# Kernel optimization log

Hardware: AMD Instinct MI355X
Metric: run time of the kernel (lower is better)

Reference implementation:

```python
import jax, jax.numpy as jnp
import numpy as np

N_NODES, IN_CH, T_IN = 2048, 64, 512
CONV_F, LSTM_H = 64, 128
NEG_BIG = -9.0e15


def conv1d(x, w, b):
    # x: [N, C_in, T], w: [C_out, C_in, 3], padding=1
    y = jax.lax.conv_general_dilated(x, w, window_strides=(1,), padding=((1, 1),),
                                     dimension_numbers=('NCH', 'OIH', 'NCH'))
    return y + b[None, :, None]


def batchnorm(x, g, b, eps=1e-5):
    # training-mode BatchNorm1d: batch stats over (N, T) per channel, biased var
    m = x.mean(axis=(0, 2), keepdims=True)
    v = x.var(axis=(0, 2), keepdims=True)
    return g[None, :, None] * (x - m) / jnp.sqrt(v + eps) + b[None, :, None]


def maxpool2(x):
    n, c, t = x.shape
    return x.reshape(n, c, t // 2, 2).max(axis=-1)


def lstm_dir(x, w_ih, w_hh, b):
    # x: [T, N, D]; gate order i, f, g, o (PyTorch convention)
    T, N, _ = x.shape
    H = w_hh.shape[1]
    pre = jnp.einsum('tnd,gd->tng', x, w_ih) + b  # [T, N, 4H]
    def step(carry, p):
        h, c = carry
        gates = p + h @ w_hh.T
        i, f, g, o = jnp.split(gates, 4, axis=-1)
        c = jax.nn.sigmoid(f) * c + jax.nn.sigmoid(i) * jnp.tanh(g)
        h = jax.nn.sigmoid(o) * jnp.tanh(c)
        return (h, c), h
    init = (jnp.zeros((N, H), x.dtype), jnp.zeros((N, H), x.dtype))
    _, hs = jax.lax.scan(step, init, pre)
    return hs  # [T, N, H]


def gat_layer(h, adj, W, a):
    # e[i,j] = leakyrelu(a . [Wh_i, Wh_j]) computed without the NxNx2F concat
    Wh = h @ W.T                      # [N, F]
    F_ = Wh.shape[1]
    s1 = Wh @ a[0, :F_]               # contribution of target node i
    s2 = Wh @ a[0, F_:]               # contribution of source node j
    e = jax.nn.leaky_relu(s1[:, None] + s2[None, :], 0.2)
    att = jax.nn.softmax(jnp.where(adj > 0, e, NEG_BIG), axis=1)
    return att @ Wh


def setup_inputs() -> dict:
    key = jax.random.key(0)
    ks = jax.random.split(key, 24)
    s = 0.05
    f32 = jnp.float32
    inp = {
        'x': jax.random.normal(ks[0], (N_NODES, IN_CH, T_IN), f32),
        'adj': jax.random.randint(ks[1], (N_NODES, N_NODES), 0, 2, jnp.int32),
        'conv1_w': s * jax.random.normal(ks[2], (CONV_F, IN_CH, 3), f32),
        'conv1_b': s * jax.random.normal(ks[3], (CONV_F,), f32),
        'bn1_g': jnp.ones((CONV_F,), f32),
        'bn1_b': jnp.zeros((CONV_F,), f32),
        'conv2_w': s * jax.random.normal(ks[4], (2 * CONV_F, CONV_F, 3), f32),
        'conv2_b': s * jax.random.normal(ks[5], (2 * CONV_F,), f32),
        'bn2_g': jnp.ones((2 * CONV_F,), f32),
        'bn2_b': jnp.zeros((2 * CONV_F,), f32),
        'wif': s * jax.random.normal(ks[6], (4 * LSTM_H, 2 * CONV_F), f32),
        'whf': s * jax.random.normal(ks[7], (4 * LSTM_H, LSTM_H), f32),
        'bf': s * jax.random.normal(ks[8], (4 * LSTM_H,), f32),
        'wir': s * jax.random.normal(ks[9], (4 * LSTM_H, 2 * CONV_F), f32),
        'whr': s * jax.random.normal(ks[10], (4 * LSTM_H, LSTM_H), f32),
        'br': s * jax.random.normal(ks[11], (4 * LSTM_H,), f32),
        'gat1_W': s * jax.random.normal(ks[12], (128, 256), f32),
        'gat1_a': s * jax.random.normal(ks[13], (1, 256), f32),
        'gat2_W': s * jax.random.normal(ks[14], (128, 128), f32),
        'gat2_a': s * jax.random.normal(ks[15], (1, 256), f32),
    }
    return inp


def reference(x, adj, conv1_w, conv1_b, bn1_g, bn1_b, conv2_w, conv2_b, bn2_g, bn2_b,
              wif, whf, bf, wir, whr, br, gat1_W, gat1_a, gat2_W, gat2_a):
    y = maxpool2(jax.nn.relu(batchnorm(conv1d(x, conv1_w, conv1_b), bn1_g, bn1_b)))
    y = maxpool2(jax.nn.relu(batchnorm(conv1d(y, conv2_w, conv2_b), bn2_g, bn2_b)))
    seq = y.transpose(2, 0, 1)                 # [T, N, 2*conv_filters]
    hf = lstm_dir(seq, wif, whf, bf)           # [T, N, H]
    hr = lstm_dir(seq[::-1], wir, whr, br)[::-1]
    feats = jnp.concatenate([hf, hr], axis=-1).mean(axis=0)  # [N, 256]
    h1 = jax.nn.elu(gat_layer(feats, adj, gat1_W, gat1_a))
    return gat_layer(h1, adj, gat2_W, gat2_a)
```

## Files before the change

kernel.cpp:

```cpp
#include <hip/hip_runtime.h>

typedef unsigned int uint;
#define DI __device__ __forceinline__

typedef __bf16 bf16;
typedef __attribute__((ext_vector_type(4))) float f32x4;
typedef __attribute__((ext_vector_type(8))) __bf16 bf16x8;
typedef __attribute__((ext_vector_type(4))) int i32x4;

constexpr size_t OFF_A    = 0;
constexpr size_t OFF_B    = 33554432;
constexpr size_t OFF_B1   = OFF_B + 16777216;
constexpr size_t OFF_WHHG = 67108864;
constexpr size_t OFF_WIHG = OFF_WHHG + 65536;
constexpr size_t OFF_BIAS = OFF_WIHG + 65536;
constexpr size_t OFF_HSUM = OFF_BIAS + 1024;
constexpr size_t OFF_FEAT = OFF_HSUM + 524288;
constexpr size_t OFF_WH1  = OFF_FEAT + 524288;
constexpr size_t OFF_S1A  = OFF_WH1 + 262144;
constexpr size_t OFF_S2A  = OFF_S1A + 2048;
constexpr size_t OFF_H1   = OFF_S2A + 2048;
constexpr size_t OFF_WH2  = OFF_H1 + 262144;
constexpr size_t OFF_S1B  = OFF_WH2 + 262144;
constexpr size_t OFF_S2B  = OFF_S1B + 2048;
constexpr size_t OFF_STAT = OFF_S2B + 2048;
constexpr size_t OFF_W1P  = OFF_STAT + 512;
constexpr size_t OFF_W2P  = OFF_W1P + 6144;
constexpr size_t OFF_WHT  = OFF_W2P + 12288;
constexpr size_t OFF_STATP= OFF_WHT + 131072;

DI float bflo(uint u){ union { uint i; float f; } v; v.i = u << 16;         return v.f; }
DI float bfhi(uint u){ union { uint i; float f; } v; v.i = u & 0xffff0000u; return v.f; }
DI float fexp2_(float x){ return __builtin_amdgcn_exp2f(x); }
DI float frcp_(float x){ return __builtin_amdgcn_rcpf(x); }
DI float sigf_(float x){ return frcp_(1.0f + fexp2_(x * -1.44269504f)); }
DI float tanhx_(float x){ return 1.0f - 2.0f*frcp_(1.0f + fexp2_(x * 2.88539009f)); }

DI f32x4 mfma16(i32x4 a, i32x4 b, f32x4 c){
  return __builtin_amdgcn_mfma_f32_16x16x32_bf16(
      __builtin_bit_cast(bf16x8, a), __builtin_bit_cast(bf16x8, b), c, 0, 0, 0);
}

DI char* swz128(char* base, int row, int byteInRow){ return base + row*128 + (byteInRow ^ ((row&7)<<4)); }
DI char* swz256(char* base, int row, int byteInRow){ return base + row*256 + (byteInRow ^ ((row&7)<<4)); }

__global__ void prep_kernel(const float* __restrict__ whf, const float* __restrict__ whr,
                            const float* __restrict__ wif, const float* __restrict__ wir,
                            const float* __restrict__ bfv, const float* __restrict__ brv,
                            const float* __restrict__ c1w, const float* __restrict__ c2w,
                            bf16* __restrict__ whh_g, bf16* __restrict__ wih_g,
                            float* __restrict__ bias_g,
                            bf16* __restrict__ w1p, bf16* __restrict__ w2p)
{
  const int dir = blockIdx.y;
  const float* whh = dir ? whr : whf;
  const float* wih = dir ? wir : wif;
  const float* bb  = dir ? brv : bfv;
  int idx = blockIdx.x*256 + threadIdx.x;
  int c = idx >> 7, d = idx & 127;
  int src = ((c & 3)*128 + (c >> 2))*128 + d;
  whh_g[(size_t)dir*65536 + idx] = (bf16)whh[src];
  wih_g[(size_t)dir*65536 + idx] = (bf16)wih[src];
  if (idx < 512) bias_g[dir*512 + idx] = bb[(idx & 3)*128 + (idx >> 2)];
  if (dir == 0) {
    if (idx < 12288) {
      int row = idx >> 6;
      int ci = (((idx & 63)*2) ^ ((row & 7) << 4)) >> 1;
      int co = row & 63, dk = row >> 6;
      w1p[idx] = (bf16)c1w[(co*64 + ci)*3 + dk];
    }
    if (idx < 24576) {
      int row = idx >> 6;
      int ci = (((idx & 63)*2) ^ ((row & 7) << 4)) >> 1;
      int co = row & 127, dk = row >> 7;
      w2p[idx] = (bf16)c2w[(co*64 + ci)*3 + dk];
    }
  }
}

__global__ __launch_bounds__(512) void conv1_kernel(
    const float* __restrict__ x, const bf16* __restrict__ w1p,
    const float* __restrict__ bias, bf16* __restrict__ y, float* __restrict__ statp)
{
  __shared__ bf16 xa[2][16512];
  __shared__ bf16 wb[12288];
  __shared__ float redS[64], redQ[64];
  const int tid = threadIdx.x, nb = blockIdx.x*8;
  {
    const i32x4* wsrc = (const i32x4*)w1p;
    for (int i = tid; i < 1536; i += 512) ((i32x4*)wb)[i] = wsrc[i];
    if (tid < 64) { redS[tid] = 0.f; redQ[tid] = 0.f; }
  }
  auto stage = [&](int buf, int n, int t0) {
    char* base = (char*)xa[buf];
    for (int i = tid; i < 2048; i += 512) {
      int q = i & 63, cp = i >> 6;
      int ci = cp*2;
      const float* xb = &x[((size_t)n*64 + ci)*512 + t0 + q*4];
      float4 v0 = *(const float4*)xb;
      float4 v1 = *(const float4*)(xb + 512);
      int row = q*4 + 1;
      union { bf16 h[2]; uint u; } p0, p1, p2, p3;
      p0.h[0]=(bf16)v0.x; p0.h[1]=(bf16)v1.x;
      p1.h[0]=(bf16)v0.y; p1.h[1]=(bf16)v1.y;
      p2.h[0]=(bf16)v0.z; p2.h[1]=(bf16)v1.z;
      p3.h[0]=(bf16)v0.w; p3.h[1]=(bf16)v1.w;
      *(uint*)swz128(base, row+0, ci*2) = p0.u;
      *(uint*)swz128(base, row+1, ci*2) = p1.u;
      *(uint*)swz128(base, row+2, ci*2) = p2.u;
      *(uint*)swz128(base, row+3, ci*2) = p3.u;
    }
    if (tid < 128) {
      int ci = tid >> 1, e = tid & 1;
      int row = e ? 257 : 0;
      int t = t0 + (e ? 256 : -1);
      float v = (t >= 0 && t < 512) ? x[((size_t)n*64 + ci)*512 + t] : 0.0f;
      *(bf16*)swz128(base, row, ci*2) = (bf16)v;
    }
  };
  stage(0, nb, 0);
  __syncthreads();
  const int lane = tid & 63, wv = tid >> 6;
  const int m0 = (wv & 3)*64, c0 = (wv >> 2)*32;
  const int l15 = lane & 15, lh = lane >> 4;
  const float bb0 = bias[c0 + l15], bb1 = bias[c0 + 16 + l15];
  float bnS[2] = {0.f,0.f}, bnQ[2] = {0.f,0.f};
  for (int it = 0; it < 16; ++it) {
    const int n = nb + (it >> 1), t0 = (it & 1)*256, buf = it & 1;
    if (it + 1 < 16) stage(buf ^ 1, nb + ((it + 1) >> 1), ((it + 1) & 1)*256);
    char* xb = (char*)xa[buf];
    f32x4 acc[4][2];
    #pragma unroll
    for (int mf = 0; mf < 4; ++mf) {
      acc[mf][0] = (f32x4){bb0, bb0, bb0, bb0};
      acc[mf][1] = (f32x4){bb1, bb1, bb1, bb1};
    }
    #pragma unroll
    for (int dk = 0; dk < 3; ++dk)
      #pragma unroll
      for (int ks = 0; ks < 2; ++ks) {
        const int kb = ks*64 + lh*16;
        i32x4 bfr[2], afr[4];
        #pragma unroll
        for (int cf = 0; cf < 2; ++cf) {
          int row = dk*64 + c0 + cf*16 + l15;
          bfr[cf] = *(const i32x4*)swz128((char*)wb, row, kb);
        }
        #pragma unroll
        for (int mf = 0; mf < 4; ++mf) {
          int row = m0 + mf*16 + l15 + dk;
          afr[mf] = *(const i32x4*)swz128(xb, row, kb);
        }
        #pragma unroll
        for (int mf = 0; mf < 4; ++mf)
          #pragma unroll
          for (int cf = 0; cf < 2; ++cf)
            acc[mf][cf] = mfma16(afr[mf], bfr[cf], acc[mf][cf]);
      }
    #pragma unroll
    for (int mf = 0; mf < 4; ++mf)
      #pragma unroll
      for (int cf = 0; cf < 2; ++cf) {
        int co = c0 + cf*16 + l15;
        int tt = t0 + m0 + mf*16 + lh*4;
        union { bf16 h[4]; uint2 u; } pk;
        #pragma unroll
        for (int r = 0; r < 4; ++r) {
          float v = acc[mf][cf][r];
          pk.h[r] = (bf16)v;
          bnS[cf] += v; bnQ[cf] += v*v;
        }
        *(uint2*)&y[((size_t)n*64 + co)*512 + tt] = pk.u;
      }
    __syncthreads();
  }
  atomicAdd(&redS[c0 + l15], bnS[0]);      atomicAdd(&redQ[c0 + l15], bnQ[0]);
  atomicAdd(&redS[c0 + 16 + l15], bnS[1]); atomicAdd(&redQ[c0 + 16 + l15], bnQ[1]);
  __syncthreads();
  if (tid < 64) {
    float* row = statp + (size_t)(blockIdx.x & 31)*256;
    atomicAdd(&row[tid], redS[tid]);
    atomicAdd(&row[128 + tid], redQ[tid]);
  }
}

__global__ __launch_bounds__(512) void conv2_kernel(
    const bf16* __restrict__ xin, const bf16* __restrict__ w2p,
    const float* __restrict__ bias, bf16* __restrict__ y, float* __restrict__ statp)
{
  __shared__ bf16 xa[2][16512];
  __shared__ bf16 wb[24576];
  __shared__ float redS[128], redQ[128];
  const int tid = threadIdx.x, nb = blockIdx.x*8;
  {
    const i32x4* wsrc = (const i32x4*)w2p;
    for (int i = tid; i < 3072; i += 512) ((i32x4*)wb)[i] = wsrc[i];
    if (tid < 128) { redS[tid] = 0.f; redQ[tid] = 0.f; }
    if (tid < 256) {
      int ci = (tid & 127) >> 1, e = tid & 1, buf = tid >> 7;
      int row = e ? 257 : 0;
      *(bf16*)swz128((char*)xa[buf], row, ci*2) = (bf16)0.0f;
    }
  }
  auto stage = [&](int buf, int n) {
    char* base = (char*)xa[buf];
    const i32x4* src = (const i32x4*)(xin + (size_t)n*16384);
    for (int i = tid; i < 2048; i += 512) {
      int row = (i >> 3) + 1, blk = i & 7;
      *(i32x4*)swz128(base, row, blk*16) = src[i];
    }
  };
  stage(0, nb);
  __syncthreads();
  const int lane = tid & 63, wv = tid >> 6;
  const int m0 = (wv & 3)*64, c0 = (wv >> 2)*64;
  const int l15 = lane & 15, lh = lane >> 4;
  float bbv[4];
  #pragma unroll
  for (int cf = 0; cf < 4; ++cf) bbv[cf] = bias[c0 + cf*16 + l15];
  float bnS[4] = {0.f,0.f,0.f,0.f}, bnQ[4] = {0.f,0.f,0.f,0.f};
  for (int it = 0; it < 8; ++it) {
    const int n = nb + it, buf = it & 1;
    if (it + 1 < 8) stage(buf ^ 1, nb + it + 1);
    char* xb = (char*)xa[buf];
    f32x4 acc[4][4];
    #pragma unroll
    for (int mf = 0; mf < 4; ++mf)
      #pragma unroll
      for (int cf = 0; cf < 4; ++cf)
        acc[mf][cf] = (f32x4){bbv[cf], bbv[cf], bbv[cf], bbv[cf]};
    #pragma unroll
    for (int dk = 0; dk < 3; ++dk)
      #pragma unroll
      for (int ks = 0; ks < 2; ++ks) {
        const int kb = ks*64 + lh*16;
        i32x4 bfr[4], afr[4];
        #pragma unroll
        for (int cf = 0; cf < 4; ++cf) {
          int row = dk*128 + c0 + cf*16 + l15;
          bfr[cf] = *(const i32x4*)swz128((char*)wb, row, kb);
        }
        #pragma unroll
        for (int mf = 0; mf < 4; ++mf) {
          int row = m0 + mf*16 + l15 + dk;
          afr[mf] = *(const i32x4*)swz128(xb, row, kb);
        }
        #pragma unroll
        for (int mf = 0; mf < 4; ++mf)
          #pragma unroll
          for (int cf = 0; cf < 4; ++cf)
            acc[mf][cf] = mfma16(afr[mf], bfr[cf], acc[mf][cf]);
      }
    #pragma unroll
    for (int mf = 0; mf < 4; ++mf)
      #pragma unroll
      for (int cf = 0; cf < 4; ++cf) {
        int co = c0 + cf*16 + l15;
        int tt = m0 + mf*16 + lh*4;
        union { bf16 h[4]; uint2 u; } pk;
        #pragma unroll
        for (int r = 0; r < 4; ++r) {
          float v = acc[mf][cf][r];
          pk.h[r] = (bf16)v;
          bnS[cf] += v; bnQ[cf] += v*v;
        }
        *(uint2*)&y[((size_t)n*128 + co)*256 + tt] = pk.u;
      }
    __syncthreads();
  }
  #pragma unroll
  for (int cf = 0; cf < 4; ++cf) {
    int co = c0 + cf*16 + l15;
    atomicAdd(&redS[co], bnS[cf]);
    atomicAdd(&redQ[co], bnQ[cf]);
  }
  __syncthreads();
  if (tid < 128) {
    float* row = statp + (size_t)(blockIdx.x & 31)*256;
    atomicAdd(&row[tid], redS[tid]);
    atomicAdd(&row[128 + tid], redQ[tid]);
  }
}

__global__ void bn_finalize_kernel(const float* __restrict__ statp, float* __restrict__ stat,
                                   const float* __restrict__ g, const float* __restrict__ b,
                                   int C, float invCnt)
{
  int c = threadIdx.x;
  if (c < C) {
    float s = 0.f, q = 0.f;
    for (int r = 0; r < 32; ++r) { s += statp[r*256 + c]; q += statp[r*256 + 128 + c]; }
    float m  = s*invCnt;
    float v  = q*invCnt - m*m;
    float sc = g[c]*rsqrtf(v + 1e-5f);
    stat[256+c] = sc;
    stat[384+c] = b[c] - m*sc;
  }
}

template<int C, int TH>
__global__ __launch_bounds__(256) void poolT_kernel(
    const bf16* __restrict__ yin, const float* __restrict__ stat, bf16* __restrict__ outp)
{
  __shared__ bf16 buf[C][TH + 2];
  const int n = blockIdx.x, tid = threadIdx.x;
  const uint* src = (const uint*)(yin + (size_t)n*C*TH*2);
  for (int i = tid; i < C*TH; i += 256) {
    int th = i & (TH - 1), c = i / TH;
    uint u = src[i];
    float sc = stat[256 + c], sh = stat[384 + c];
    float a = fmaxf(sc*bflo(u) + sh, 0.f);
    float b = fmaxf(sc*bfhi(u) + sh, 0.f);
    buf[c][th] = (bf16)fmaxf(a, b);
  }
  __syncthreads();
  bf16* dst = outp + (size_t)n*TH*C;
  for (int i = tid; i < TH*C/2; i += 256) {
    int cp = i & (C/2 - 1), th = i / (C/2);
    union { bf16 h[2]; uint u; } pk;
    pk.h[0] = buf[2*cp][th]; pk.h[1] = buf[2*cp + 1][th];
    *(uint*)&dst[th*C + 2*cp] = pk.u;
  }
}

__global__ __launch_bounds__(512, 2) void lstm_fused_kernel(
    const bf16* __restrict__ p2t, const bf16* __restrict__ wih_g,
    const bf16* __restrict__ whh_g, const float* __restrict__ bias_g,
    float* __restrict__ hsum)
{
  __shared__ bf16 hb[2][2048];
  const int z = blockIdx.x;
  const int dir = z & 1, n0 = (z >> 1)*16;
  const int tid = threadIdx.x, lane = tid & 63, wv = tid >> 6;
  const int l15 = lane & 15, lh = lane >> 4;
  i32x4 wihr[4][4], whhr[4][4];
  {
    const bf16* wi = wih_g + (size_t)dir*65536;
    const bf16* wh = whh_g + (size_t)dir*65536;
    #pragma unroll
    for (int cf = 0; cf < 4; ++cf) {
      int c = wv*64 + cf*16 + l15;
      #pragma unroll
      for (int ks = 0; ks < 4; ++ks) {
        wihr[cf][ks] = *(const i32x4*)(wi + (size_t)c*128 + ks*32 + lh*8);
        whhr[cf][ks] = *(const i32x4*)(wh + (size_t)c*128 + ks*32 + lh*8);
      }
    }
  }
  f32x4 bias4[4];
  #pragma unroll
  for (int cf = 0; cf < 4; ++cf) {
    int hh = wv*16 + cf*4 + lh;
    bias4[cf] = *(const f32x4*)&bias_g[dir*512 + hh*4];
  }
  for (int i = tid; i < 256; i += 512) ((i32x4*)hb[0])[i] = (i32x4){0,0,0,0};
  const bf16* xrow = p2t + (size_t)(n0 + l15)*128*128;
  float creg[4] = {0.f,0.f,0.f,0.f}, hac[4] = {0.f,0.f,0.f,0.f};
  f32x4 acc[4];
  i32x4 xn[4];
  {
    int ts0 = dir ? 127 : 0;
    #pragma unroll
    for (int ks = 0; ks < 4; ++ks)
      xn[ks] = *(const i32x4*)(xrow + (size_t)ts0*128 + ks*32 + lh*8);
    #pragma unroll
    for (int cf = 0; cf < 4; ++cf) {
      acc[cf] = mfma16(wihr[cf][0], xn[0], bias4[cf]);
      #pragma unroll
      for (int ks = 1; ks < 4; ++ks)
        acc[cf] = mfma16(wihr[cf][ks], xn[ks], acc[cf]);
    }
  }
  int cur = 0;
  __syncthreads();
  for (int t = 0; t < 128; ++t) {
    {
      int tn = (t + 1 < 128) ? t + 1 : 127;
      int tsn = dir ? 127 - tn : tn;
      #pragma unroll
      for (int ks = 0; ks < 4; ++ks)
        xn[ks] = *(const i32x4*)(xrow + (size_t)tsn*128 + ks*32 + lh*8);
    }
    {
      i32x4 a0 = *(const i32x4*)swz256((char*)hb[cur], l15, 0*64 + lh*16);
      i32x4 a1 = *(const i32x4*)swz256((char*)hb[cur], l15, 1*64 + lh*16);
      #pragma unroll
      for (int cf = 0; cf < 4; ++cf) {
        acc[cf] = mfma16(whhr[cf][0], a0, acc[cf]);
        acc[cf] = mfma16(whhr[cf][1], a1, acc[cf]);
      }
      a0 = *(const i32x4*)swz256((char*)hb[cur], l15, 2*64 + lh*16);
      a1 = *(const i32x4*)swz256((char*)hb[cur], l15, 3*64 + lh*16);
      #pragma unroll
      for (int cf = 0; cf < 4; ++cf) {
        acc[cf] = mfma16(whhr[cf][2], a0, acc[cf]);
        acc[cf] = mfma16(whhr[cf][3], a1, acc[cf]);
      }
    }
    #pragma unroll
    for (int cf = 0; cf < 4; ++cf) {
      float ig = sigf_(acc[cf][0]);
      float fg = sigf_(acc[cf][1]);
      float gg = tanhx_(acc[cf][2]);
      float og = sigf_(acc[cf][3]);
      float cv = fg*creg[cf] + ig*gg;
      creg[cf] = cv;
      float hv = og*tanhx_(cv);
      hac[cf] += hv;
      int hh = wv*16 + cf*4 + lh;
      *(bf16*)swz256((char*)hb[cur^1], l15, hh*2) = (bf16)hv;
    }
    #pragma unroll
    for (int cf = 0; cf < 4; ++cf) {
      acc[cf] = mfma16(wihr[cf][0], xn[0], bias4[cf]);
      #pragma unroll
      for (int ks = 1; ks < 4; ++ks)
        acc[cf] = mfma16(wihr[cf][ks], xn[ks], acc[cf]);
    }
    __syncthreads();
    cur ^= 1;
  }
  float* hm = hsum + ((size_t)dir*2048 + n0)*128;
  #pragma unroll
  for (int cf = 0; cf < 4; ++cf) {
    int hh = wv*16 + cf*4 + lh;
    hm[(size_t)l15*128 + hh] = hac[cf];
  }
}

__global__ __launch_bounds__(256) void feats_kernel(const float* __restrict__ hsum, float* __restrict__ feats)
{
  int idx = blockIdx.x*256 + threadIdx.x;
  int k = idx & 255, n = idx >> 8;
  float v = (k < 128) ? hsum[(size_t)n*128 + k]
                      : hsum[(size_t)2048*128 + (size_t)n*128 + (k - 128)];
  feats[idx] = v * 0.0078125f;
}

template<int K>
__global__ __launch_bounds__(256) void node_gemm_kernel(
    const float* __restrict__ inp, const float* __restrict__ W,
    float* __restrict__ outp, bf16* __restrict__ outT)
{
  __shared__ float ft[32][K];
  const int i0 = blockIdx.x*32, tid = threadIdx.x;
  for (int i = tid; i < 32*K; i += 256) ft[i/K][i%K] = inp[(size_t)i0*K + i];
  __syncthreads();
  const int f = tid & 127, ih = (tid >> 7)*16;
  float acc[16];
  #pragma unroll
  for (int ii = 0; ii < 16; ++ii) acc[ii] = 0.f;
  const float* wp = W + (size_t)f*K;
  for (int k = 0; k < K; k += 4) {
    const float4 wv = *reinterpret_cast<const float4*>(&wp[k]);
    #pragma unroll
    for (int ii = 0; ii < 16; ++ii) {
      const float* fp = &ft[ih+ii][k];
      acc[ii] += fp[0]*wv.x + fp[1]*wv.y + fp[2]*wv.z + fp[3]*wv.w;
    }
  }
  union { bf16 h[16]; uint4 u[2]; } pk;
  #pragma unroll
  for (int ii = 0; ii < 16; ++ii) {
    outp[(size_t)(i0+ih+ii)*128 + f] = acc[ii];
    pk.h[ii] = (bf16)acc[ii];
  }
  uint4* dT = (uint4*)&outT[(size_t)f*2048 + i0 + ih];
  dT[0] = pk.u[0]; dT[1] = pk.u[1];
}

__global__ __launch_bounds__(256) void gat_s_kernel(const float* __restrict__ Wh,
    const float* __restrict__ a, float* __restrict__ s1, float* __restrict__ s2)
{
  const int node = blockIdx.x*4 + (threadIdx.x >> 6);
  const int l = threadIdx.x & 63;
  const float w0 = Wh[(size_t)node*128 + l], w1 = Wh[(size_t)node*128 + 64 + l];
  float v1 = w0*a[l]     + w1*a[64+l];
  float v2 = w0*a[128+l] + w1*a[192+l];
  #pragma unroll
  for (int off = 32; off > 0; off >>= 1) { v1 += __shfl_down(v1, off); v2 += __shfl_down(v2, off); }
  if (l == 0) { s1[node] = v1; s2[node] = v2; }
}

__global__ __launch_bounds__(512) void gat_attn8_kernel(
    const bf16* __restrict__ WhT,
    const float* __restrict__ s1, const float* __restrict__ s2v,
    const int* __restrict__ adj, float* __restrict__ outp, int applyElu)
{
  __shared__ bf16 P[8*2048];
  __shared__ float sums[8];
  const int i0 = blockIdx.x*8, tid = threadIdx.x;
  const int lane = tid & 63, w = tid >> 6;
  {
    const int r = w, i = i0 + r;
    const float s1i = s1[i];
    const int4* arow = (const int4*)(adj + (size_t)i*2048);
    float ev[8][4];
    float m = -3.0e38f;
    #pragma unroll
    for (int k = 0; k < 8; ++k) {
      int4 ad = arow[k*64 + lane];
      float4 sv = *(const float4*)&s2v[k*256 + lane*4];
      float e0 = s1i + sv.x; e0 = (e0 > 0.f) ? e0 : 0.2f*e0; e0 = (ad.x > 0) ? e0 : -3.0e38f;
      float e1 = s1i + sv.y; e1 = (e1 > 0.f) ? e1 : 0.2f*e1; e1 = (ad.y > 0) ? e1 : -3.0e38f;
      float e2 = s1i + sv.z; e2 = (e2 > 0.f) ? e2 : 0.2f*e2; e2 = (ad.z > 0) ? e2 : -3.0e38f;
      float e3 = s1i + sv.w; e3 = (e3 > 0.f) ? e3 : 0.2f*e3; e3 = (ad.w > 0) ? e3 : -3.0e38f;
      ev[k][0]=e0; ev[k][1]=e1; ev[k][2]=e2; ev[k][3]=e3;
      m = fmaxf(m, fmaxf(fmaxf(e0,e1), fmaxf(e2,e3)));
    }
    #pragma unroll
    for (int off = 32; off > 0; off >>= 1) m = fmaxf(m, __shfl_xor(m, off));
    float s = 0.f;
    char* prow = (char*)P + r*4096;
    #pragma unroll
    for (int k = 0; k < 8; ++k) {
      float p0 = __expf(ev[k][0] - m);
      float p1 = __expf(ev[k][1] - m);
      float p2 = __expf(ev[k][2] - m);
      float p3 = __expf(ev[k][3] - m);
      s += (p0+p1)+(p2+p3);
      union { bf16 h[4]; uint2 u; } pk;
      pk.h[0]=(bf16)p0; pk.h[1]=(bf16)p1; pk.h[2]=(bf16)p2; pk.h[3]=(bf16)p3;
      *(uint2*)(prow + ((k*512 + lane*8) ^ ((r&7)<<4))) = pk.u;
    }
    #pragma unroll
    for (int off = 32; off > 0; off >>= 1) s += __shfl_xor(s, off);
    if (lane == 0) sums[r] = s;
  }
  __syncthreads();
  const int l15 = lane & 15, lh = lane >> 4;
  const int pr = l15 & 7;
  const bf16* bT = WhT + (size_t)(w*16 + l15)*2048;
  f32x4 ac[4];
  #pragma unroll
  for (int q = 0; q < 4; ++q) ac[q] = (f32x4){0.f,0.f,0.f,0.f};
  for (int kt = 0; kt < 64; kt += 4) {
    #pragma unroll
    for (int q = 0; q < 4; ++q) {
      i32x4 af = *(const i32x4*)((char*)P + pr*4096 + (((kt+q)*64 + lh*16) ^ ((pr&7)<<4)));
      i32x4 bf = *(const i32x4*)(bT + (kt+q)*32 + lh*8);
      ac[q] = mfma16(af, bf, ac[q]);
    }
  }
  f32x4 accv = (ac[0] + ac[1]) + (ac[2] + ac[3]);
  if (lh < 2) {
    #pragma unroll
    for (int rg = 0; rg < 4; ++rg) {
      int row = lh*4 + rg;
      float v = accv[rg] / sums[row];
      if (applyElu) v = (v > 0.f) ? v : (__expf(v) - 1.0f);
      outp[(size_t)(i0 + row)*128 + w*16 + l15] = v;
    }
  }
}

extern "C" void kernel_launch(void* const* d_in, const int* in_sizes, int n_in,
                              void* d_out, int out_size, void* d_ws, size_t ws_size,
                              hipStream_t stream)
{
  (void)in_sizes; (void)n_in; (void)out_size; (void)ws_size;
  const float* x    = (const float*)d_in[0];
  const int*   adj  = (const int*)d_in[1];
  const float* c1w  = (const float*)d_in[2];
  const float* c1b  = (const float*)d_in[3];
  const float* bn1g = (const float*)d_in[4];
  const float* bn1b = (const float*)d_in[5];
  const float* c2w  = (const float*)d_in[6];
  const float* c2b  = (const float*)d_in[7];
  const float* bn2g = (const float*)d_in[8];
  const float* bn2b = (const float*)d_in[9];
  const float* wif  = (const float*)d_in[10];
  const float* whf  = (const float*)d_in[11];
  const float* bfv  = (const float*)d_in[12];
  const float* wir  = (const float*)d_in[13];
  const float* whr  = (const float*)d_in[14];
  const float* brv  = (const float*)d_in[15];
  const float* g1W  = (const float*)d_in[16];
  const float* g1a  = (const float*)d_in[17];
  const float* g2W  = (const float*)d_in[18];
  const float* g2a  = (const float*)d_in[19];
  float* outp = (float*)d_out;
  float* ws   = (float*)d_ws;

  bf16* y12    = (bf16*)(ws + OFF_A);
  bf16* pool1t = (bf16*)(ws + OFF_B);
  bf16* pool2t = (bf16*)(ws + OFF_B1);
  bf16* whh_g  = (bf16*)(ws + OFF_WHHG);
  bf16* wih_g  = (bf16*)(ws + OFF_WIHG);
  float* bias_g= ws + OFF_BIAS;
  float* hsm   = ws + OFF_HSUM;
  float* feats = ws + OFF_FEAT;
  float* Wh1   = ws + OFF_WH1;
  float* s1a   = ws + OFF_S1A;
  float* s2a   = ws + OFF_S2A;
  float* h1    = ws + OFF_H1;
  float* Wh2   = ws + OFF_WH2;
  float* s1b   = ws + OFF_S1B;
  float* s2b   = ws + OFF_S2B;
  float* stat  = ws + OFF_STAT;
  bf16* w1p    = (bf16*)(ws + OFF_W1P);
  bf16* w2p    = (bf16*)(ws + OFF_W2P);
  bf16* whT    = (bf16*)(ws + OFF_WHT);
  float* statp = ws + OFF_STATP;

  prep_kernel<<<dim3(256,2),256,0,stream>>>(whf, whr, wif, wir, bfv, brv, c1w, c2w,
                                            whh_g, wih_g, bias_g, w1p, w2p);

  hipMemsetAsync(statp, 0, 8192*sizeof(float), stream);
  conv1_kernel<<<256,512,0,stream>>>(x, w1p, c1b, y12, statp);
  bn_finalize_kernel<<<1,128,0,stream>>>(statp, stat, bn1g, bn1b, 64, 1.0f/(2048.0f*512.0f));
  poolT_kernel<64,256><<<2048,256,0,stream>>>(y12, stat, pool1t);

  hipMemsetAsync(statp, 0, 8192*sizeof(float), stream);
  conv2_kernel<<<256,512,0,stream>>>(pool1t, w2p, c2b, y12, statp);
  bn_finalize_kernel<<<1,128,0,stream>>>(statp, stat, bn2g, bn2b, 128, 1.0f/(2048.0f*256.0f));
  poolT_kernel<128,128><<<2048,256,0,stream>>>(y12, stat, pool2t);

  lstm_fused_kernel<<<256,512,0,stream>>>(pool2t, wih_g, whh_g, bias_g, hsm);
  feats_kernel<<<2048,256,0,stream>>>(hsm, feats);

  node_gemm_kernel<256><<<64,256,0,stream>>>(feats, g1W, Wh1, whT);
  gat_s_kernel<<<512,256,0,stream>>>(Wh1, g1a, s1a, s2a);
  gat_attn8_kernel<<<256,512,0,stream>>>(whT, s1a, s2a, adj, h1, 1);
  node_gemm_kernel<128><<<64,256,0,stream>>>(h1, g2W, Wh2, whT);
  gat_s_kernel<<<512,256,0,stream>>>(Wh2, g2a, s1b, s2b);
  gat_attn8_kernel<<<256,512,0,stream>>>(whT, s1b, s2b, adj, outp, 0);
}
```

Baseline: 558.6 us.

## Fuse BN1, ReLU, maxpool and transpose into conv2 input staging

```diff
diff --git a/kernel.cpp b/kernel.cpp
--- a/kernel.cpp
+++ b/kernel.cpp
@@ -10,7 +10,6 @@
 
 constexpr size_t OFF_A    = 0;
 constexpr size_t OFF_B    = 33554432;
-constexpr size_t OFF_B1   = OFF_B + 16777216;
 constexpr size_t OFF_WHHG = 67108864;
 constexpr size_t OFF_WIHG = OFF_WHHG + 65536;
 constexpr size_t OFF_BIAS = OFF_WIHG + 65536;
@@ -185,8 +184,9 @@
 }
 
 __global__ __launch_bounds__(512) void conv2_kernel(
-    const bf16* __restrict__ xin, const bf16* __restrict__ w2p,
-    const float* __restrict__ bias, bf16* __restrict__ y, float* __restrict__ statp)
+    const bf16* y1, const bf16* __restrict__ w2p,
+    const float* __restrict__ bias, const float* __restrict__ stat,
+    bf16* y, float* __restrict__ statp)
 {
   __shared__ bf16 xa[2][16512];
   __shared__ bf16 wb[24576];
@@ -204,10 +204,18 @@
   }
   auto stage = [&](int buf, int n) {
     char* base = (char*)xa[buf];
-    const i32x4* src = (const i32x4*)(xin + (size_t)n*16384);
-    for (int i = tid; i < 2048; i += 512) {
-      int row = (i >> 3) + 1, blk = i & 7;
-      *(i32x4*)swz128(base, row, blk*16) = src[i];
+    for (int i = tid; i < 8192; i += 512) {
+      int t = i & 255, cp = i >> 8;
+      int ci = cp*2;
+      uint u0 = *(const uint*)&y1[((size_t)n*64 + ci    )*512 + 2*t];
+      uint u1 = *(const uint*)&y1[((size_t)n*64 + ci + 1)*512 + 2*t];
+      float sc0 = stat[256 + ci],     sh0 = stat[384 + ci];
+      float sc1 = stat[256 + ci + 1], sh1 = stat[384 + ci + 1];
+      float a0 = fmaxf(fmaxf(sc0*bflo(u0) + sh0, 0.f), fmaxf(sc0*bfhi(u0) + sh0, 0.f));
+      float a1 = fmaxf(fmaxf(sc1*bflo(u1) + sh1, 0.f), fmaxf(sc1*bfhi(u1) + sh1, 0.f));
+      union { bf16 h[2]; uint u; } pk;
+      pk.h[0] = (bf16)a0; pk.h[1] = (bf16)a1;
+      *(uint*)swz128(base, t + 1, ci*2) = pk.u;
     }
   };
   stage(0, nb);
@@ -582,9 +590,9 @@
   float* outp = (float*)d_out;
   float* ws   = (float*)d_ws;
 
-  bf16* y12    = (bf16*)(ws + OFF_A);
-  bf16* pool1t = (bf16*)(ws + OFF_B);
-  bf16* pool2t = (bf16*)(ws + OFF_B1);
+  bf16* y1     = (bf16*)(ws + OFF_A);
+  bf16* y2     = (bf16*)(ws + OFF_B);
+  bf16* pool2t = (bf16*)(ws + OFF_A);
   bf16* whh_g  = (bf16*)(ws + OFF_WHHG);
   bf16* wih_g  = (bf16*)(ws + OFF_WIHG);
   float* bias_g= ws + OFF_BIAS;
@@ -607,14 +615,13 @@
                                             whh_g, wih_g, bias_g, w1p, w2p);
 
   hipMemsetAsync(statp, 0, 8192*sizeof(float), stream);
-  conv1_kernel<<<256,512,0,stream>>>(x, w1p, c1b, y12, statp);
+  conv1_kernel<<<256,512,0,stream>>>(x, w1p, c1b, y1, statp);
   bn_finalize_kernel<<<1,128,0,stream>>>(statp, stat, bn1g, bn1b, 64, 1.0f/(2048.0f*512.0f));
-  poolT_kernel<64,256><<<2048,256,0,stream>>>(y12, stat, pool1t);
 
   hipMemsetAsync(statp, 0, 8192*sizeof(float), stream);
-  conv2_kernel<<<256,512,0,stream>>>(pool1t, w2p, c2b, y12, statp);
+  conv2_kernel<<<256,512,0,stream>>>(y1, w2p, c2b, stat, y2, statp);
   bn_finalize_kernel<<<1,128,0,stream>>>(statp, stat, bn2g, bn2b, 128, 1.0f/(2048.0f*256.0f));
-  poolT_kernel<128,128><<<2048,256,0,stream>>>(y12, stat, pool2t);
+  poolT_kernel<128,128><<<2048,256,0,stream>>>(y2, stat, pool2t);
 
   lstm_fused_kernel<<<256,512,0,stream>>>(pool2t, wih_g, whh_g, bias_g, hsm);
   feats_kernel<<<2048,256,0,stream>>>(hsm, feats);
```

After: 564.2 us. Within noise of the previous version (+1.0%).
